# Kernel optimization log

Hardware: AMD Instinct MI355X
Metric: run time of the kernel (lower is better)

Reference implementation:

```python
import jax, jax.numpy as jnp
import numpy as np

B, SEQ, NF = 16, 512, 32
E, HID, PRED = 128, 512, 96
N_FFT, HOP, TOPM = 64, 32, 32
W = SEQ // HOP + 1          # 17 windows (centered STFT)
F = N_FFT // 2 + 1          # 33 onesided freqs
LAM = 0.01                  # sparsity_threshold (softshrink)
SCALE = 0.02


def _hann(n):
    # periodic hann, matches torch.hann_window default
    return 0.5 - 0.5 * jnp.cos(2.0 * jnp.pi * jnp.arange(n) / n)


def _softshrink(v):
    return jnp.sign(v) * jnp.maximum(jnp.abs(v) - LAM, 0.0)


def setup_inputs():
    key = jax.random.key(0)
    ks = jax.random.split(key, 12)
    d = {}
    d['x'] = jax.random.normal(ks[0], (B, SEQ, NF), jnp.float32)
    d['embeddings'] = jax.random.normal(ks[1], (1, E), jnp.float32)
    for nm, k in zip(['Wr', 'Wi', 'Wrl', 'Wil', 'Wrr', 'Wir'], ks[2:8]):
        d[nm] = SCALE * jax.random.normal(k, (W, E, E), jnp.float32)
    d['br'] = SCALE * jax.random.normal(ks[8], (W, E), jnp.float32)
    d['bi'] = SCALE * jax.random.normal(ks[9], (W, E), jnp.float32)
    d['fc_w1'] = SCALE * jax.random.normal(ks[10], (SEQ * E, HID), jnp.float32)
    d['fc_b1'] = jnp.zeros((HID,), jnp.float32)
    d['fc_w2'] = SCALE * jax.random.normal(ks[11], (HID, PRED), jnp.float32)
    d['fc_b2'] = jnp.zeros((PRED,), jnp.float32)
    return d


def _forward(x, embeddings, Wr, Wi, Wrl, Wil, Wrr, Wir, br, bi,
             fc_w1, fc_b1, fc_w2, fc_b2):
    Bq, T, N = x.shape
    # tokenEmb: (B,T,N) -> (B,N,T,E)
    xe = x.transpose(0, 2, 1)[..., None] * embeddings
    bias = xe
    # ---- STFT (centered, reflect pad, hann, onesided) ----
    xt = xe.transpose(0, 1, 3, 2)                      # (B,N,E,T)
    pad = N_FFT // 2
    xp = jnp.pad(xt, ((0, 0), (0, 0), (0, 0), (pad, pad)), mode='reflect')
    win = _hann(N_FFT).astype(x.dtype)
    idx = jnp.arange(W)[:, None] * HOP + jnp.arange(N_FFT)[None, :]  # (W,nfft)
    frames = xp[..., idx] * win                        # (B,N,E,W,nfft)
    spec = jnp.fft.rfft(frames, axis=-1)               # (B,N,E,W,F)
    spec = spec.transpose(0, 1, 3, 4, 2)               # (B,N,W,F,E)
    # ---- top-M frequency select (dim=3) ----
    sm = jnp.moveaxis(spec, 3, -1)                     # (B,N,W,E,F)
    _, top_idx = jax.lax.top_k(jnp.abs(sm), TOPM)      # (B,N,W,E,M)
    vals = jnp.take_along_axis(sm, top_idx, axis=-1)
    xw = jnp.moveaxis(vals, -1, 3)                     # (B,N,W,M,E)
    # ---- per-window complex MLP with left/right neighbor windows ----
    z0 = jnp.zeros_like(xw[:, :, :1])
    xl = jnp.concatenate([z0, xw[:, :, :-1]], axis=2)  # left neighbor (zero at w=0)
    xr = jnp.concatenate([xw[:, :, 1:], z0], axis=2)   # right neighbor (zero at w=W-1)

    def cmul(z, wr, wi):
        re = jnp.einsum('bnwme,wef->bnwmf', z.real, wr) - jnp.einsum('bnwme,wef->bnwmf', z.imag, wi)
        im = jnp.einsum('bnwme,wef->bnwmf', z.imag, wr) + jnp.einsum('bnwme,wef->bnwmf', z.real, wi)
        return re, im

    re_m, im_m = cmul(xw, Wr, Wi)
    re_l, im_l = cmul(xl, Wrl, Wil)
    re_r, im_r = cmul(xr, Wrr, Wir)
    o_re = jax.nn.relu(re_m + re_l + re_r + br[None, None, :, None, :])
    o_im = jax.nn.relu(im_m + im_l + im_r + bi[None, None, :, None, :])
    y = _softshrink(o_re) + 1j * _softshrink(o_im)     # (B,N,W,M,E) complex
    # ---- scatter-pad back to full frequency grid ----
    ym = jnp.moveaxis(y, 3, -1)                        # (B,N,W,E,M)
    K = Bq * N * W * E
    flat_vals = ym.reshape(K, TOPM)
    flat_idx = top_idx.reshape(K, TOPM)
    full = jnp.zeros((K, F), ym.dtype).at[jnp.arange(K)[:, None], flat_idx].set(flat_vals)
    spec_full = jnp.moveaxis(full.reshape(Bq, N, W, E, F), -1, 3)  # (B,N,W,F,E)
    # ---- ISTFT (windowed OLA / window-squared envelope, centered trim) ----
    sf = spec_full.transpose(0, 1, 4, 2, 3)            # (B,N,E,W,F)
    fr = jnp.fft.irfft(sf, n=N_FFT, axis=-1) * win     # (B,N,E,W,nfft)
    L = (W - 1) * HOP + N_FFT
    ola = jnp.zeros((Bq, N, E, L), fr.dtype).at[..., idx].add(fr)
    env = jnp.zeros((L,), win.dtype).at[idx].add(win * win)
    ola = ola / jnp.where(env > 1e-11, env, 1.0)
    xt2 = ola[..., pad:L - pad]                        # (B,N,E,T)
    xo = xt2.transpose(0, 1, 3, 2) + bias              # (B,N,T,E) + residual
    # ---- fc head ----
    h = xo.reshape(Bq, N, T * E)
    h = jax.nn.leaky_relu(h @ fc_w1 + fc_b1, 0.01)
    out = h @ fc_w2 + fc_b2                            # (B,N,PRED)
    return out.transpose(0, 2, 1)                      # (B,PRED,N)


def reference(x, embeddings, Wr, Wi, Wrl, Wil, Wrr, Wir, br, bi,
              fc_w1, fc_b1, fc_w2, fc_b2):
    return _forward(x, embeddings, Wr, Wi, Wrl, Wil, Wrr, Wir, br, bi,
                    fc_w1, fc_b1, fc_w2, fc_b2)
```

## Files before the change

kernel.cpp:

```cpp
#include <hip/hip_runtime.h>
#include <hip/hip_bf16.h>

#define LAM 0.01f

typedef __attribute__((ext_vector_type(8))) short v8s;
typedef __attribute__((ext_vector_type(4))) float v4f;

static __device__ __forceinline__ unsigned short f2bf(float f) {
    union { float f; unsigned int u; } v; v.f = f;
    unsigned int u = v.u;
    u += 0x7fffu + ((u >> 16) & 1u);
    return (unsigned short)(u >> 16);
}
static __device__ __forceinline__ float bf2f(unsigned short h) {
    union { unsigned int u; float f; } c; c.u = ((unsigned int)h) << 16;
    return c.f;
}
static __device__ __forceinline__ unsigned int pkbf(float a, float b) {
    union { __hip_bfloat162 h; unsigned int u; } c;
    c.h = __float22bfloat162_rn(float2{a, b});
    return c.u;
}

static __device__ __forceinline__ void async16(const void* g, void* l) {
    __builtin_amdgcn_global_load_lds(
        (const __attribute__((address_space(1))) unsigned int*)g,
        (__attribute__((address_space(3))) unsigned int*)l, 16, 0, 0);
}

#define OFF_COEF 0ull
#define OFF_V    69632ull
#define OFF_BINS 2297856ull
#define OFF_AIMG 3411968ull
#define OFF_W1P  70520832ull
#define OFF_HP   137629696ull

__global__ __launch_bounds__(256) void pre_kernel(
    const float* __restrict__ w1, unsigned short* __restrict__ w1p,
    const float* __restrict__ emb,
    const float* __restrict__ Wr, const float* __restrict__ Wi,
    const float* __restrict__ Wrl, const float* __restrict__ Wil,
    const float* __restrict__ Wrr, const float* __restrict__ Wir,
    const float* __restrict__ br, const float* __restrict__ bi,
    float* __restrict__ coef)
{
    if (blockIdx.y == 4) {
        const int bx = blockIdx.x;
        if (bx >= 68) return;
        const int pair = bx * 2 + (threadIdx.x >> 7);
        const int w = pair >> 3, j = pair & 7, e = threadIdx.x & 127;
        float out;
        if (j < 6) {
            const float* Wj;
            switch (j) {
                case 0: Wj = Wr; break; case 1: Wj = Wi; break;
                case 2: Wj = Wrl; break; case 3: Wj = Wil; break;
                case 4: Wj = Wrr; break; default: Wj = Wir; break;
            }
            const float* p = Wj + (size_t)w * 16384 + e;
            float acc = 0.f;
            #pragma unroll 8
            for (int ep = 0; ep < 128; ++ep) acc = fmaf(emb[ep], p[ep * 128], acc);
            out = acc;
        } else if (j == 6) {
            out = br[w * 128 + e] - LAM;
        } else {
            out = bi[w * 128 + e] - LAM;
        }
        coef[((size_t)(w * 128 + e)) * 8 + j] = out;
        return;
    }

    __shared__ float T[32][132];
    const int kb = blockIdx.x, nt = blockIdx.y;
    const int tid = threadIdx.x;

    #pragma unroll
    for (int p = 0; p < 4; ++p) {
        int r = (tid >> 5) + p * 8;
        int c = (tid & 31) * 4;
        float4 v = *(const float4*)&w1[((size_t)(kb * 32 + r)) * 512 + nt * 128 + c];
        T[r][c] = v.x; T[r][c + 1] = v.y; T[r][c + 2] = v.z; T[r][c + 3] = v.w;
    }
    __syncthreads();

    unsigned short* dst = w1p + ((size_t)nt * 2048 + kb) * 4096;
    #pragma unroll
    for (int p = 0; p < 2; ++p) {
        int pos = tid + 256 * p;
        int np = pos >> 2, cs = pos & 3;
        int clog = cs ^ ((np >> 2) & 3);
        unsigned int pk[4];
        #pragma unroll
        for (int j2 = 0; j2 < 4; ++j2)
            pk[j2] = pkbf(T[clog * 8 + j2 * 2][np], T[clog * 8 + j2 * 2 + 1][np]);
        *(uint4*)&dst[pos * 8] = make_uint4(pk[0], pk[1], pk[2], pk[3]);
    }
}

__global__ __launch_bounds__(256) void stft_kernel(
    const float* __restrict__ x, float2* __restrict__ V, int* __restrict__ bins)
{
    __shared__ float sig[576];
    __shared__ float winT[64];
    __shared__ float2 tw[64];
    __shared__ float2 Sbuf[17 * 33];
    __shared__ float absb[17 * 33];

    const int blk = blockIdx.x;
    const int b = blk >> 5, n = blk & 31;
    const int tid = threadIdx.x;
    const float C64 = 0.09817477042468103f;

    if (tid < 64) {
        float ang = (float)tid * C64;
        winT[tid] = 0.5f - 0.5f * cosf(ang);
        tw[tid] = make_float2(cosf(ang), sinf(ang));
    }
    for (int l = tid; l < 576; l += 256) {
        int t = (l < 32) ? (32 - l) : ((l < 544) ? (l - 32) : (1054 - l));
        sig[l] = x[(size_t)b * 16384 + t * 32 + n];
    }
    __syncthreads();

    for (int task = tid; task < 561; task += 256) {
        int w = task / 33, f = task - w * 33;
        float sr = 0.f, si = 0.f;
        int base = w * 32;
        for (int t = 0; t < 64; ++t) {
            float sw = sig[base + t] * winT[t];
            float2 cs = tw[(f * t) & 63];
            sr = fmaf(sw, cs.x, sr);
            si = fmaf(sw, -cs.y, si);
        }
        Sbuf[task] = make_float2(sr, si);
        absb[task] = sqrtf(fmaf(sr, sr, si * si));
    }
    __syncthreads();

    for (int task = tid; task < 561; task += 256) {
        int w = task / 33, f = task - w * 33;
        float a = absb[task];
        int base = w * 33, rank = 0;
        for (int j = 0; j < 33; ++j) {
            float aj = absb[base + j];
            rank += (aj > a) || (aj == a && j < f);
        }
        if (rank < 32) {
            size_t o = ((size_t)blk * 17 + w) * 32 + rank;
            V[o] = Sbuf[task];
            bins[o] = f;
        }
    }
}

#define MID_ROLL(J0, J1, J2, J3)                                                \
    {                                                                           \
        _Pragma("unroll") for (int e2 = 0; e2 < 2; ++e2)                        \
        _Pragma("unroll") for (int i = 0; i < 4; ++i) {                         \
            roll[e2][J0][i] = fmaf(acc[0][e2][i], win16[0][i], roll[e2][J0][i]);\
            roll[e2][J1][i] = fmaf(acc[1][e2][i], win16[1][i], roll[e2][J1][i]);\
            roll[e2][J2][i] = fmaf(acc[2][e2][i], win16[2][i], roll[e2][J2][i]);\
            roll[e2][J3][i] = fmaf(acc[3][e2][i], win16[3][i], roll[e2][J3][i]);\
        }                                                                       \
    }

#define MID_FLUSH(JJA, JJB)                                                     \
    {                                                                           \
        _Pragma("unroll") for (int i = 0; i < 4; ++i) {                         \
            int tp = 32 * (w - 1) + q * 4 + i;                                  \
            float xb = xs[tp];                                                  \
            _Pragma("unroll") for (int e2 = 0; e2 < 2; ++e2) {                  \
                float val = fmaf(roll[e2][JJA][i], renv[0][i], xb * emb2[e2]);  \
                Aimg[cbase[e2] + (size_t)tp * 16384] = f2bf(val);               \
                roll[e2][JJA][i] = 0.f;                                         \
            }                                                                   \
            int tp2 = tp + 16;                                                  \
            float xb2 = xs[tp2];                                                \
            _Pragma("unroll") for (int e2 = 0; e2 < 2; ++e2) {                  \
                float val = fmaf(roll[e2][JJB][i], renv[1][i], xb2 * emb2[e2]); \
                Aimg[cbase[e2] + (size_t)tp2 * 16384] = f2bf(val);              \
                roll[e2][JJB][i] = 0.f;                                         \
            }                                                                   \
        }                                                                       \
    }

__global__ __launch_bounds__(256, 4) void mid_kernel(
    const float* __restrict__ x, const float* __restrict__ emb,
    const float* __restrict__ coef, const float2* __restrict__ V,
    const int* __restrict__ bins, unsigned short* __restrict__ Aimg)
{
    __shared__ unsigned short M1t[64 * 72];
    __shared__ unsigned short Yt[128 * 72];
    __shared__ float cosT[64];
    __shared__ float sinT[64];
    __shared__ float2 Vs2[19 * 32];
    __shared__ int Bns[17 * 32];
    __shared__ float xs[512];

    const int blk = blockIdx.x;
    const int b = blk >> 5, n = blk & 31;
    const int tid = threadIdx.x;
    const int wave = tid >> 6, lane = tid & 63, l15 = lane & 15, q = lane >> 4;
    const float C64 = 0.09817477042468103f;

    if (tid < 64) {
        float ang = (float)tid * C64;
        cosT[tid] = __cosf(ang);
        sinT[tid] = __sinf(ang);
    }
    {
        const float2* Vg = V + (size_t)blk * 544;
        const int* Bg = bins + (size_t)blk * 544;
        for (int i = tid; i < 544; i += 256) { Vs2[32 + i] = Vg[i]; Bns[i] = Bg[i]; }
        if (tid < 64) {
            int r = (tid < 32) ? tid : (18 * 32 + tid - 32);
            Vs2[r] = make_float2(0.f, 0.f);
        }
        for (int i = tid; i < 512; i += 256) xs[i] = x[(size_t)b * 16384 + i * 32 + n];
    }

    float win16[4][4];
    #pragma unroll
    for (int tt = 0; tt < 4; ++tt)
        #pragma unroll
        for (int i = 0; i < 4; ++i) {
            int t = tt * 16 + q * 4 + i;
            win16[tt][i] = 0.5f - 0.5f * __cosf((float)t * C64);
        }
    float renv[2][4];
    #pragma unroll
    for (int hf = 0; hf < 2; ++hf)
        #pragma unroll
        for (int i = 0; i < 4; ++i) {
            int k = hf * 16 + q * 4 + i;
            float w0 = 0.5f - 0.5f * __cosf((float)k * C64);
            float w1v = 0.5f - 0.5f * __cosf((float)(k + 32) * C64);
            renv[hf][i] = 1.0f / (w0 * w0 + w1v * w1v);
        }
    int ebase[2];
    float emb2[2];
    size_t cbase[2];
    const int mt = blk >> 7, mp = blk & 127, s = (mp >> 2) & 3;
    #pragma unroll
    for (int e2 = 0; e2 < 2; ++e2) {
        ebase[e2] = (wave * 2 + e2) * 16 + l15;
        emb2[e2] = emb[ebase[e2]];
        int e = ebase[e2];
        int echunk = e >> 5, clog = (e >> 3) & 3, cs = clog ^ s, el = e & 7;
        cbase[e2] = ((size_t)mt * 2048 + echunk) * 4096 + mp * 32 + cs * 8 + el;
    }

    float roll[2][4][4];
    #pragma unroll
    for (int e2 = 0; e2 < 2; ++e2)
        #pragma unroll
        for (int jj = 0; jj < 4; ++jj)
            #pragma unroll
            for (int i = 0; i < 4; ++i) roll[e2][jj][i] = 0.f;

    const int e1 = tid & 127;
    const int mg = (tid >> 7) << 4;
    const int tM = tid & 63;
    const int kg = wave << 4;

    __syncthreads();

    for (int w = 0; w < 17; ++w) {
        {
            const float4* cf = (const float4*)(coef + ((size_t)(w * 128 + e1)) * 8);
            float4 cA = cf[0];
            float4 cB = cf[1];
            #pragma unroll
            for (int half = 0; half < 2; ++half) {
                unsigned int rep[4], imp[4];
                #pragma unroll
                for (int j2 = 0; j2 < 4; ++j2) {
                    float rev[2], imv[2];
                    #pragma unroll
                    for (int sdx = 0; sdx < 2; ++sdx) {
                        int m = mg + half * 8 + j2 * 2 + sdx;
                        float2 vm = Vs2[(w + 1) * 32 + m];
                        float2 vl = Vs2[w * 32 + m];
                        float2 vp = Vs2[(w + 2) * 32 + m];
                        float re = cB.z;
                        re = fmaf(vm.x, cA.x, re); re = fmaf(-vm.y, cA.y, re);
                        re = fmaf(vl.x, cA.z, re); re = fmaf(-vl.y, cA.w, re);
                        re = fmaf(vp.x, cB.x, re); re = fmaf(-vp.y, cB.y, re);
                        float im = cB.w;
                        im = fmaf(vm.y, cA.x, im); im = fmaf(vm.x, cA.y, im);
                        im = fmaf(vl.y, cA.z, im); im = fmaf(vl.x, cA.w, im);
                        im = fmaf(vp.y, cB.x, im); im = fmaf(vp.x, cB.y, im);
                        rev[sdx] = fmaxf(re, 0.f);
                        imv[sdx] = fmaxf(im, 0.f);
                    }
                    rep[j2] = pkbf(rev[0], rev[1]);
                    imp[j2] = pkbf(imv[0], imv[1]);
                }
                ((uint4*)&Yt[e1 * 72 + mg])[half] =
                    make_uint4(rep[0], rep[1], rep[2], rep[3]);
                ((uint4*)&Yt[e1 * 72 + 32 + mg])[half] =
                    make_uint4(imp[0], imp[1], imp[2], imp[3]);
            }
        }
        {
            #pragma unroll
            for (int half = 0; half < 2; ++half) {
                unsigned int mpk[4];
                #pragma unroll
                for (int j2 = 0; j2 < 4; ++j2) {
                    float vv[2];
                    #pragma unroll
                    for (int sdx = 0; sdx < 2; ++sdx) {
                        int k = kg + half * 8 + j2 * 2 + sdx;
                        int m = k & 31;
                        int r = Bns[w * 32 + m];
                        float sc = (r == 0 || r == 32) ? 0.015625f : 0.03125f;
                        int idx = (r * tM) & 63;
                        vv[sdx] = (k < 32) ? (cosT[idx] * sc) : (-sinT[idx] * sc);
                    }
                    mpk[j2] = pkbf(vv[0], vv[1]);
                }
                ((uint4*)&M1t[tM * 72 + kg])[half] =
                    make_uint4(mpk[0], mpk[1], mpk[2], mpk[3]);
            }
        }
        __syncthreads();

        v4f acc[4][2];
        #pragma unroll
        for (int tt = 0; tt < 4; ++tt)
            #pragma unroll
            for (int e2 = 0; e2 < 2; ++e2) acc[tt][e2] = (v4f){0.f, 0.f, 0.f, 0.f};
        #pragma unroll
        for (int ks = 0; ks < 2; ++ks) {
            v8s bfr[2];
            #pragma unroll
            for (int e2 = 0; e2 < 2; ++e2)
                bfr[e2] = *(const v8s*)&Yt[ebase[e2] * 72 + ks * 32 + q * 8];
            #pragma unroll
            for (int tt = 0; tt < 4; ++tt) {
                v8s af = *(const v8s*)&M1t[(tt * 16 + l15) * 72 + ks * 32 + q * 8];
                #pragma unroll
                for (int e2 = 0; e2 < 2; ++e2)
                    acc[tt][e2] = __builtin_amdgcn_mfma_f32_16x16x32_bf16(
                        af, bfr[e2], acc[tt][e2], 0, 0, 0);
            }
        }

        if ((w & 1) == 0) {
            MID_ROLL(0, 1, 2, 3);
            if (w > 0) {
                MID_FLUSH(0, 1);
            } else {
                #pragma unroll
                for (int e2 = 0; e2 < 2; ++e2)
                    #pragma unroll
                    for (int i = 0; i < 4; ++i) {
                        roll[e2][0][i] = 0.f; roll[e2][1][i] = 0.f;
                    }
            }
        } else {
            MID_ROLL(2, 3, 0, 1);
            MID_FLUSH(2, 3);
        }
        if (w < 16) __syncthreads();
    }
}

__global__ __launch_bounds__(512) void gemm_kernel(
    const unsigned short* __restrict__ Aimg, const unsigned short* __restrict__ w1p,
    unsigned short* __restrict__ hp, int iters, int KS)
{
    __shared__ unsigned short As[3][8192];
    __shared__ unsigned short Bs[3][8192];

    const int gid = blockIdx.x;
    const int xcd = gid & 7;
    const int u = gid >> 3;
    const int KS4 = KS >> 2;
    const int nt2 = (u >= KS4) ? 1 : 0;
    const int vv = u - nt2 * KS4;
    const int pid = vv * 8 + xcd;
    const int ks = pid >> 1;
    const int mt2 = pid & 1;

    const int tid = threadIdx.x;
    const int wave = tid >> 6, lane = tid & 63;
    const int l15 = lane & 15, q = lane >> 4;
    const int kb0 = ks * iters;

    const int isB = wave >> 2;
    const int sub = wave & 3;
    const unsigned short* gsrc = (isB
        ? w1p + ((size_t)(nt2 * 2 + (sub >> 1)) * 2048 + kb0) * 4096
        : Aimg + ((size_t)(mt2 * 2 + (sub >> 1)) * 2048 + kb0) * 4096)
        + (sub & 1) * 2048 + lane * 8;
    const int ldsoff = (sub >> 1) * 4096 + (sub & 1) * 2048;

    v4f acc[4][8];
    #pragma unroll
    for (int mf = 0; mf < 4; ++mf)
        #pragma unroll
        for (int nf = 0; nf < 8; ++nf) acc[mf][nf] = (v4f){0.f, 0.f, 0.f, 0.f};

    {
        unsigned short* dst0 = (isB ? Bs[0] : As[0]) + ldsoff;
        #pragma unroll
        for (int j = 0; j < 4; ++j) async16(gsrc + j * 512, dst0 + j * 512);
        if (iters > 1) {
            const unsigned short* s1 = gsrc + 4096;
            unsigned short* dst1 = (isB ? Bs[1] : As[1]) + ldsoff;
            #pragma unroll
            for (int j = 0; j < 4; ++j) async16(s1 + j * 512, dst1 + j * 512);
        }
    }

    const int wm = wave >> 1, wn = wave & 1;
    const int ca = (q ^ ((l15 >> 2) & 3)) * 8;
    const int rA = (wm >> 1) * 4096 + ((wm & 1) * 64 + l15) * 32 + ca;
    const int rB = wn * 4096 + l15 * 32 + ca;

    for (int it = 0; it < iters; ++it) {
        if (it + 1 < iters) {
            asm volatile("s_waitcnt vmcnt(4)" ::: "memory");
        } else {
            asm volatile("s_waitcnt vmcnt(0)" ::: "memory");
        }
        __builtin_amdgcn_s_barrier();
        __builtin_amdgcn_sched_barrier(0);
        if (it + 2 < iters) {
            const int nb = (it + 2) % 3;
            const unsigned short* src = gsrc + (size_t)(it + 2) * 4096;
            unsigned short* dst = (isB ? Bs[nb] : As[nb]) + ldsoff;
            #pragma unroll
            for (int j = 0; j < 4; ++j) async16(src + j * 512, dst + j * 512);
        }
        const int cur = it % 3;
        v8s af[4], bf[8];
        #pragma unroll
        for (int f = 0; f < 4; ++f) af[f] = *(const v8s*)&As[cur][rA + f * 512];
        #pragma unroll
        for (int nf = 0; nf < 8; ++nf) bf[nf] = *(const v8s*)&Bs[cur][rB + nf * 512];
        #pragma unroll
        for (int mf = 0; mf < 4; ++mf)
            #pragma unroll
            for (int nf = 0; nf < 8; ++nf)
                acc[mf][nf] = __builtin_amdgcn_mfma_f32_16x16x32_bf16(
                    af[mf], bf[nf], acc[mf][nf], 0, 0, 0);
    }

    #pragma unroll
    for (int mf = 0; mf < 4; ++mf)
        #pragma unroll
        for (int nf = 0; nf < 8; ++nf) {
            int row = mt2 * 256 + wm * 64 + mf * 16 + q * 4;
            int col = nt2 * 256 + wn * 128 + nf * 16 + l15;
            unsigned short* dst = hp + ((size_t)row * KS + ks) * 512 + col;
            #pragma unroll
            for (int i = 0; i < 4; ++i)
                dst[(size_t)i * KS * 512] = f2bf(acc[mf][nf][i]);
        }
}

__global__ __launch_bounds__(256) void fc2_kernel(
    const unsigned short* __restrict__ hp, const float* __restrict__ b1,
    const float* __restrict__ w2, const float* __restrict__ b2,
    float* __restrict__ out, int KS)
{
    __shared__ float hbuf[512];
    __shared__ float part[2][96];
    const int row = blockIdx.x;
    const int tid = threadIdx.x;

    const unsigned int* base = (const unsigned int*)(hp + (size_t)row * KS * 512) + tid;
    float a0 = 0.f, a1 = 0.f;
    #pragma unroll 8
    for (int k = 0; k < KS; ++k) {
        unsigned int v = base[k * 256];
        a0 += bf2f((unsigned short)(v & 0xffff));
        a1 += bf2f((unsigned short)(v >> 16));
    }
    float s0 = a0 + b1[tid * 2];
    float s1 = a1 + b1[tid * 2 + 1];
    hbuf[tid * 2]     = (s0 > 0.f) ? s0 : 0.01f * s0;
    hbuf[tid * 2 + 1] = (s1 > 0.f) ? s1 : 0.01f * s1;
    __syncthreads();

    if (tid < 192) {
        const int c = (tid >= 96) ? 1 : 0;
        const int o = tid - 96 * c;
        float a = 0.f;
        #pragma unroll 8
        for (int h = c * 256; h < c * 256 + 256; ++h)
            a = fmaf(hbuf[h], w2[h * 96 + o], a);
        part[c][o] = a;
    }
    __syncthreads();

    if (tid < 96) {
        float a = part[0][tid] + part[1][tid] + b2[tid];
        int b = row >> 5, n = row & 31;
        out[(size_t)b * 3072 + tid * 32 + n] = a;
    }
}

extern "C" void kernel_launch(void* const* d_in, const int* in_sizes, int n_in,
                              void* d_out, int out_size, void* d_ws, size_t ws_size,
                              hipStream_t stream) {
    const float* x   = (const float*)d_in[0];
    const float* emb = (const float*)d_in[1];
    const float* Wr  = (const float*)d_in[2];
    const float* Wi  = (const float*)d_in[3];
    const float* Wrl = (const float*)d_in[4];
    const float* Wil = (const float*)d_in[5];
    const float* Wrr = (const float*)d_in[6];
    const float* Wir = (const float*)d_in[7];
    const float* br  = (const float*)d_in[8];
    const float* bi  = (const float*)d_in[9];
    const float* w1  = (const float*)d_in[10];
    const float* b1  = (const float*)d_in[11];
    const float* w2  = (const float*)d_in[12];
    const float* b2  = (const float*)d_in[13];

    char* ws = (char*)d_ws;
    float* coef          = (float*)(ws + OFF_COEF);
    float2* V            = (float2*)(ws + OFF_V);
    int* bins            = (int*)(ws + OFF_BINS);
    unsigned short* Aimg = (unsigned short*)(ws + OFF_AIMG);
    unsigned short* w1p  = (unsigned short*)(ws + OFF_W1P);
    unsigned short* hpp  = (unsigned short*)(ws + OFF_HP);

    int KS = 64;
    size_t hp_bytes = (size_t)KS * 512 * 512 * 2;
    if (OFF_HP + hp_bytes > ws_size) {
        KS = 32; hp_bytes = (size_t)KS * 512 * 512 * 2;
    }
    int iters = 2048 / KS;

    pre_kernel<<<dim3(2048, 5), dim3(256), 0, stream>>>(
        w1, w1p, emb, Wr, Wi, Wrl, Wil, Wrr, Wir, br, bi, coef);
    stft_kernel<<<dim3(512), dim3(256), 0, stream>>>(x, V, bins);
    mid_kernel<<<dim3(512), dim3(256), 0, stream>>>(x, emb, coef, V, bins, Aimg);
    gemm_kernel<<<dim3(4 * KS), dim3(512), 0, stream>>>(Aimg, w1p, hpp, iters, KS);
    fc2_kernel<<<dim3(512), dim3(256), 0, stream>>>(hpp, b1, w2, b2, (float*)d_out, KS);
}
```

Baseline: 398.8 us.

## Split STFT and mid kernels across two blocks per series, double-buffer LDS

The STFT kernel now splits the 17 windows of each (batch, feature) series across two blocks (9 + 8). The mid kernel splits the 128 embedding channels into two halves of 64, so both launch 1024 blocks instead of 512. The mid kernel also double-buffers its Yt/M1t shared tiles by window parity, which drops the trailing barrier per window iteration. The aim is more parallelism and occupancy on a GPU with many CUs. The cost is recomputing the DFT basis matrix M1t, and reloading V/bins and x, in both halves.

```diff
diff --git a/kernel.cpp b/kernel.cpp
--- a/kernel.cpp
+++ b/kernel.cpp
@@ -101,14 +101,19 @@
 __global__ __launch_bounds__(256) void stft_kernel(
     const float* __restrict__ x, float2* __restrict__ V, int* __restrict__ bins)
 {
-    __shared__ float sig[576];
+    __shared__ float sigL[336];
     __shared__ float winT[64];
     __shared__ float2 tw[64];
-    __shared__ float2 Sbuf[17 * 33];
-    __shared__ float absb[17 * 33];
+    __shared__ float2 Sbuf[9 * 33];
+    __shared__ float absb[9 * 33];
 
     const int blk = blockIdx.x;
-    const int b = blk >> 5, n = blk & 31;
+    const int bn = blk >> 1, wh = blk & 1;
+    const int b = bn >> 5, n = bn & 31;
+    const int w0 = wh ? 9 : 0;
+    const int nW = wh ? 8 : 9;
+    const int sbase = wh ? 288 : 0;
+    const int slen = wh ? 288 : 320;
     const int tid = threadIdx.x;
     const float C64 = 0.09817477042468103f;
 
@@ -117,18 +122,20 @@
         winT[tid] = 0.5f - 0.5f * cosf(ang);
         tw[tid] = make_float2(cosf(ang), sinf(ang));
     }
-    for (int l = tid; l < 576; l += 256) {
-        int t = (l < 32) ? (32 - l) : ((l < 544) ? (l - 32) : (1054 - l));
-        sig[l] = x[(size_t)b * 16384 + t * 32 + n];
+    for (int l = tid; l < slen; l += 256) {
+        int g = sbase + l;
+        int t = (g < 32) ? (32 - g) : ((g < 544) ? (g - 32) : (1054 - g));
+        sigL[l] = x[(size_t)b * 16384 + t * 32 + n];
     }
     __syncthreads();
 
-    for (int task = tid; task < 561; task += 256) {
-        int w = task / 33, f = task - w * 33;
+    const int ntask = nW * 33;
+    for (int task = tid; task < ntask; task += 256) {
+        int wl = task / 33, f = task - wl * 33;
         float sr = 0.f, si = 0.f;
-        int base = w * 32;
+        int base = (w0 + wl) * 32 - sbase;
         for (int t = 0; t < 64; ++t) {
-            float sw = sig[base + t] * winT[t];
+            float sw = sigL[base + t] * winT[t];
             float2 cs = tw[(f * t) & 63];
             sr = fmaf(sw, cs.x, sr);
             si = fmaf(sw, -cs.y, si);
@@ -138,16 +145,16 @@
     }
     __syncthreads();
 
-    for (int task = tid; task < 561; task += 256) {
-        int w = task / 33, f = task - w * 33;
+    for (int task = tid; task < ntask; task += 256) {
+        int wl = task / 33, f = task - wl * 33;
         float a = absb[task];
-        int base = w * 33, rank = 0;
+        int base = wl * 33, rank = 0;
         for (int j = 0; j < 33; ++j) {
             float aj = absb[base + j];
             rank += (aj > a) || (aj == a && j < f);
         }
         if (rank < 32) {
-            size_t o = ((size_t)blk * 17 + w) * 32 + rank;
+            size_t o = ((size_t)bn * 17 + (w0 + wl)) * 32 + rank;
             V[o] = Sbuf[task];
             bins[o] = f;
         }
@@ -156,12 +163,11 @@
 
 #define MID_ROLL(J0, J1, J2, J3)                                                \
     {                                                                           \
-        _Pragma("unroll") for (int e2 = 0; e2 < 2; ++e2)                        \
         _Pragma("unroll") for (int i = 0; i < 4; ++i) {                         \
-            roll[e2][J0][i] = fmaf(acc[0][e2][i], win16[0][i], roll[e2][J0][i]);\
-            roll[e2][J1][i] = fmaf(acc[1][e2][i], win16[1][i], roll[e2][J1][i]);\
-            roll[e2][J2][i] = fmaf(acc[2][e2][i], win16[2][i], roll[e2][J2][i]);\
-            roll[e2][J3][i] = fmaf(acc[3][e2][i], win16[3][i], roll[e2][J3][i]);\
+            roll[J0][i] = fmaf(acc[0][i], win16[0][i], roll[J0][i]);            \
+            roll[J1][i] = fmaf(acc[1][i], win16[1][i], roll[J1][i]);            \
+            roll[J2][i] = fmaf(acc[2][i], win16[2][i], roll[J2][i]);            \
+            roll[J3][i] = fmaf(acc[3][i], win16[3][i], roll[J3][i]);            \
         }                                                                       \
     }
 
@@ -170,18 +176,14 @@
         _Pragma("unroll") for (int i = 0; i < 4; ++i) {                         \
             int tp = 32 * (w - 1) + q * 4 + i;                                  \
             float xb = xs[tp];                                                  \
-            _Pragma("unroll") for (int e2 = 0; e2 < 2; ++e2) {                  \
-                float val = fmaf(roll[e2][JJA][i], renv[0][i], xb * emb2[e2]);  \
-                Aimg[cbase[e2] + (size_t)tp * 16384] = f2bf(val);               \
-                roll[e2][JJA][i] = 0.f;                                         \
-            }                                                                   \
+            float val = fmaf(roll[JJA][i], renv[0][i], xb * emb2v);             \
+            Aimg[cbase + (size_t)tp * 16384] = f2bf(val);                       \
+            roll[JJA][i] = 0.f;                                                 \
             int tp2 = tp + 16;                                                  \
             float xb2 = xs[tp2];                                                \
-            _Pragma("unroll") for (int e2 = 0; e2 < 2; ++e2) {                  \
-                float val = fmaf(roll[e2][JJB][i], renv[1][i], xb2 * emb2[e2]); \
-                Aimg[cbase[e2] + (size_t)tp2 * 16384] = f2bf(val);              \
-                roll[e2][JJB][i] = 0.f;                                         \
-            }                                                                   \
+            float val2 = fmaf(roll[JJB][i], renv[1][i], xb2 * emb2v);           \
+            Aimg[cbase + (size_t)tp2 * 16384] = f2bf(val2);                     \
+            roll[JJB][i] = 0.f;                                                 \
         }                                                                       \
     }
 
@@ -190,8 +192,8 @@
     const float* __restrict__ coef, const float2* __restrict__ V,
     const int* __restrict__ bins, unsigned short* __restrict__ Aimg)
 {
-    __shared__ unsigned short M1t[64 * 72];
-    __shared__ unsigned short Yt[128 * 72];
+    __shared__ unsigned short M1t[2][64 * 72];
+    __shared__ unsigned short Yt[2][64 * 72];
     __shared__ float cosT[64];
     __shared__ float sinT[64];
     __shared__ float2 Vs2[19 * 32];
@@ -199,7 +201,8 @@
     __shared__ float xs[512];
 
     const int blk = blockIdx.x;
-    const int b = blk >> 5, n = blk & 31;
+    const int bn = blk >> 1, eh = blk & 1;
+    const int b = bn >> 5, n = bn & 31;
     const int tid = threadIdx.x;
     const int wave = tid >> 6, lane = tid & 63, l15 = lane & 15, q = lane >> 4;
     const float C64 = 0.09817477042468103f;
@@ -210,8 +213,8 @@
         sinT[tid] = __sinf(ang);
     }
     {
-        const float2* Vg = V + (size_t)blk * 544;
-        const int* Bg = bins + (size_t)blk * 544;
+        const float2* Vg = V + (size_t)bn * 544;
+        const int* Bg = bins + (size_t)bn * 544;
         for (int i = tid; i < 544; i += 256) { Vs2[32 + i] = Vg[i]; Bns[i] = Bg[i]; }
         if (tid < 64) {
             int r = (tid < 32) ? tid : (18 * 32 + tid - 32);
@@ -238,113 +241,97 @@
             float w1v = 0.5f - 0.5f * __cosf((float)(k + 32) * C64);
             renv[hf][i] = 1.0f / (w0 * w0 + w1v * w1v);
         }
-    int ebase[2];
-    float emb2[2];
-    size_t cbase[2];
-    const int mt = blk >> 7, mp = blk & 127, s = (mp >> 2) & 3;
-    #pragma unroll
-    for (int e2 = 0; e2 < 2; ++e2) {
-        ebase[e2] = (wave * 2 + e2) * 16 + l15;
-        emb2[e2] = emb[ebase[e2]];
-        int e = ebase[e2];
-        int echunk = e >> 5, clog = (e >> 3) & 3, cs = clog ^ s, el = e & 7;
-        cbase[e2] = ((size_t)mt * 2048 + echunk) * 4096 + mp * 32 + cs * 8 + el;
-    }
-
-    float roll[2][4][4];
-    #pragma unroll
-    for (int e2 = 0; e2 < 2; ++e2)
-        #pragma unroll
-        for (int jj = 0; jj < 4; ++jj)
-            #pragma unroll
-            for (int i = 0; i < 4; ++i) roll[e2][jj][i] = 0.f;
-
-    const int e1 = tid & 127;
-    const int mg = (tid >> 7) << 4;
+
+    const int ebl = wave * 16 + l15;
+    const int eg = eh * 64 + ebl;
+    const float emb2v = emb[eg];
+    size_t cbase;
+    {
+        const int mt = bn >> 7, mp = bn & 127, s = (mp >> 2) & 3;
+        int echunk = eg >> 5, clog = (eg >> 3) & 3, cs = clog ^ s, el = eg & 7;
+        cbase = ((size_t)mt * 2048 + echunk) * 4096 + mp * 32 + cs * 8 + el;
+    }
+
+    float roll[4][4];
+    #pragma unroll
+    for (int jj = 0; jj < 4; ++jj)
+        #pragma unroll
+        for (int i = 0; i < 4; ++i) roll[jj][i] = 0.f;
+
+    const int e1l = tid & 63;
+    const int eg1 = eh * 64 + e1l;
+    const int mg = (tid >> 6) * 8;
     const int tM = tid & 63;
-    const int kg = wave << 4;
+    const int kg = (tid >> 6) * 16;
 
     __syncthreads();
 
     for (int w = 0; w < 17; ++w) {
+        const int buf = w & 1;
         {
-            const float4* cf = (const float4*)(coef + ((size_t)(w * 128 + e1)) * 8);
+            const float4* cf = (const float4*)(coef + ((size_t)(w * 128 + eg1)) * 8);
             float4 cA = cf[0];
             float4 cB = cf[1];
-            #pragma unroll
-            for (int half = 0; half < 2; ++half) {
-                unsigned int rep[4], imp[4];
+            unsigned int rep[4], imp[4];
+            #pragma unroll
+            for (int j2 = 0; j2 < 4; ++j2) {
+                float rev[2], imv[2];
                 #pragma unroll
-                for (int j2 = 0; j2 < 4; ++j2) {
-                    float rev[2], imv[2];
-                    #pragma unroll
-                    for (int sdx = 0; sdx < 2; ++sdx) {
-                        int m = mg + half * 8 + j2 * 2 + sdx;
-                        float2 vm = Vs2[(w + 1) * 32 + m];
-                        float2 vl = Vs2[w * 32 + m];
-                        float2 vp = Vs2[(w + 2) * 32 + m];
-                        float re = cB.z;
-                        re = fmaf(vm.x, cA.x, re); re = fmaf(-vm.y, cA.y, re);
-                        re = fmaf(vl.x, cA.z, re); re = fmaf(-vl.y, cA.w, re);
-                        re = fmaf(vp.x, cB.x, re); re = fmaf(-vp.y, cB.y, re);
-                        float im = cB.w;
-                        im = fmaf(vm.y, cA.x, im); im = fmaf(vm.x, cA.y, im);
-                        im = fmaf(vl.y, cA.z, im); im = fmaf(vl.x, cA.w, im);
-                        im = fmaf(vp.y, cB.x, im); im = fmaf(vp.x, cB.y, im);
-                        rev[sdx] = fmaxf(re, 0.f);
-                        imv[sdx] = fmaxf(im, 0.f);
-                    }
-                    rep[j2] = pkbf(rev[0], rev[1]);
-                    imp[j2] = pkbf(imv[0], imv[1]);
+                for (int sdx = 0; sdx < 2; ++sdx) {
+                    int m = mg + j2 * 2 + sdx;
+                    float2 vm = Vs2[(w + 1) * 32 + m];
+                    float2 vl = Vs2[w * 32 + m];
+                    float2 vp = Vs2[(w + 2) * 32 + m];
+                    float re = cB.z;
+                    re = fmaf(vm.x, cA.x, re); re = fmaf(-vm.y, cA.y, re);
+                    re = fmaf(vl.x, cA.z, re); re = fmaf(-vl.y, cA.w, re);
+                    re = fmaf(vp.x, cB.x, re); re = fmaf(-vp.y, cB.y, re);
+                    float im = cB.w;
+                    im = fmaf(vm.y, cA.x, im); im = fmaf(vm.x, cA.y, im);
+                    im = fmaf(vl.y, cA.z, im); im = fmaf(vl.x, cA.w, im);
+                    im = fmaf(vp.y, cB.x, im); im = fmaf(vp.x, cB.y, im);
+                    rev[sdx] = fmaxf(re, 0.f);
+                    imv[sdx] = fmaxf(im, 0.f);
                 }
-                ((uint4*)&Yt[e1 * 72 + mg])[half] =
-                    make_uint4(rep[0], rep[1], rep[2], rep[3]);
-                ((uint4*)&Yt[e1 * 72 + 32 + mg])[half] =
-                    make_uint4(imp[0], imp[1], imp[2], imp[3]);
+                rep[j2] = pkbf(rev[0], rev[1]);
+                imp[j2] = pkbf(imv[0], imv[1]);
             }
+            *(uint4*)&Yt[buf][e1l * 72 + mg]      = make_uint4(rep[0], rep[1], rep[2], rep[3]);
+            *(uint4*)&Yt[buf][e1l * 72 + 32 + mg] = make_uint4(imp[0], imp[1], imp[2], imp[3]);
         }
         {
-            #pragma unroll
-            for (int half = 0; half < 2; ++half) {
-                unsigned int mpk[4];
+            unsigned int mpk[8];
+            #pragma unroll
+            for (int j2 = 0; j2 < 8; ++j2) {
+                float vv[2];
                 #pragma unroll
-                for (int j2 = 0; j2 < 4; ++j2) {
-                    float vv[2];
-                    #pragma unroll
-                    for (int sdx = 0; sdx < 2; ++sdx) {
-                        int k = kg + half * 8 + j2 * 2 + sdx;
-                        int m = k & 31;
-                        int r = Bns[w * 32 + m];
-                        float sc = (r == 0 || r == 32) ? 0.015625f : 0.03125f;
-                        int idx = (r * tM) & 63;
-                        vv[sdx] = (k < 32) ? (cosT[idx] * sc) : (-sinT[idx] * sc);
-                    }
-                    mpk[j2] = pkbf(vv[0], vv[1]);
+                for (int sdx = 0; sdx < 2; ++sdx) {
+                    int k = kg + j2 * 2 + sdx;
+                    int m = k & 31;
+                    int r = Bns[w * 32 + m];
+                    float sc = (r == 0 || r == 32) ? 0.015625f : 0.03125f;
+                    int idx = (r * tM) & 63;
+                    vv[sdx] = (k < 32) ? (cosT[idx] * sc) : (-sinT[idx] * sc);
                 }
-                ((uint4*)&M1t[tM * 72 + kg])[half] =
-                    make_uint4(mpk[0], mpk[1], mpk[2], mpk[3]);
+                mpk[j2] = pkbf(vv[0], vv[1]);
             }
+            uint4* dm = (uint4*)&M1t[buf][tM * 72 + kg];
+            dm[0] = make_uint4(mpk[0], mpk[1], mpk[2], mpk[3]);
+            dm[1] = make_uint4(mpk[4], mpk[5], mpk[6], mpk[7]);
         }
         __syncthreads();
 
-        v4f acc[4][2];
-        #pragma unroll
-        for (int tt = 0; tt < 4; ++tt)
-            #pragma unroll
-            for (int e2 = 0; e2 < 2; ++e2) acc[tt][e2] = (v4f){0.f, 0.f, 0.f, 0.f};
+        v4f acc[4];
+        #pragma unroll
+        for (int tt = 0; tt < 4; ++tt) acc[tt] = (v4f){0.f, 0.f, 0.f, 0.f};
         #pragma unroll
         for (int ks = 0; ks < 2; ++ks) {
-            v8s bfr[2];
-            #pragma unroll
-            for (int e2 = 0; e2 < 2; ++e2)
-                bfr[e2] = *(const v8s*)&Yt[ebase[e2] * 72 + ks * 32 + q * 8];
+            v8s bfr = *(const v8s*)&Yt[buf][ebl * 72 + ks * 32 + q * 8];
             #pragma unroll
             for (int tt = 0; tt < 4; ++tt) {
-                v8s af = *(const v8s*)&M1t[(tt * 16 + l15) * 72 + ks * 32 + q * 8];
-                #pragma unroll
-                for (int e2 = 0; e2 < 2; ++e2)
-                    acc[tt][e2] = __builtin_amdgcn_mfma_f32_16x16x32_bf16(
-                        af, bfr[e2], acc[tt][e2], 0, 0, 0);
+                v8s af = *(const v8s*)&M1t[buf][(tt * 16 + l15) * 72 + ks * 32 + q * 8];
+                acc[tt] = __builtin_amdgcn_mfma_f32_16x16x32_bf16(
+                    af, bfr, acc[tt], 0, 0, 0);
             }
         }
 
@@ -354,17 +341,12 @@
                 MID_FLUSH(0, 1);
             } else {
                 #pragma unroll
-                for (int e2 = 0; e2 < 2; ++e2)
-                    #pragma unroll
-                    for (int i = 0; i < 4; ++i) {
-                        roll[e2][0][i] = 0.f; roll[e2][1][i] = 0.f;
-                    }
+                for (int i = 0; i < 4; ++i) { roll[0][i] = 0.f; roll[1][i] = 0.f; }
             }
         } else {
             MID_ROLL(2, 3, 0, 1);
             MID_FLUSH(2, 3);
         }
-        if (w < 16) __syncthreads();
     }
 }
 
@@ -540,8 +522,8 @@
 
     pre_kernel<<<dim3(2048, 5), dim3(256), 0, stream>>>(
         w1, w1p, emb, Wr, Wi, Wrl, Wil, Wrr, Wir, br, bi, coef);
-    stft_kernel<<<dim3(512), dim3(256), 0, stream>>>(x, V, bins);
-    mid_kernel<<<dim3(512), dim3(256), 0, stream>>>(x, emb, coef, V, bins, Aimg);
+    stft_kernel<<<dim3(1024), dim3(256), 0, stream>>>(x, V, bins);
+    mid_kernel<<<dim3(1024), dim3(256), 0, stream>>>(x, emb, coef, V, bins, Aimg);
     gemm_kernel<<<dim3(4 * KS), dim3(512), 0, stream>>>(Aimg, w1p, hpp, iters, KS);
     fc2_kernel<<<dim3(512), dim3(256), 0, stream>>>(hpp, b1, w2, b2, (float*)d_out, KS);
 }
```

Measured after the change: 409.0 us. 2.6% more time.
